# Kernel optimization log

Measured on AMD Instinct MI355X. Metric: run time of the kernel, lower is better.

## Reference

```python
import jax, jax.numpy as jnp
import numpy as np

B, T, E, D, OUT = 2048, 64, 256, 256, 2


def setup_inputs() -> dict:
    key = jax.random.key(0)
    ks = jax.random.split(key, 16)
    s = 0.05
    return {
        "input_encoded": jax.random.normal(ks[0], (B, T, E), dtype=jnp.float32),
        "y_history": jax.random.normal(ks[1], (B, T), dtype=jnp.float32),
        # attn_layer: Linear(2D+E -> E), Tanh, Linear(E -> 1)
        "W1": jax.random.normal(ks[2], (E, 2 * D + E), dtype=jnp.float32) * s,
        "b1": jax.random.normal(ks[3], (E,), dtype=jnp.float32) * s,
        "w2": jax.random.normal(ks[4], (E,), dtype=jnp.float32) * s,
        "b2": jax.random.normal(ks[5], (1,), dtype=jnp.float32) * s,
        # single-layer LSTM(input=OUT, hidden=D); gate order i,f,g,o
        "W_ih": jax.random.normal(ks[6], (4 * D, OUT), dtype=jnp.float32) * s,
        "b_ih": jax.random.normal(ks[7], (4 * D,), dtype=jnp.float32) * s,
        "W_hh": jax.random.normal(ks[8], (4 * D, D), dtype=jnp.float32) * s,
        "b_hh": jax.random.normal(ks[9], (4 * D,), dtype=jnp.float32) * s,
        # fc: Linear(E+T -> OUT) (torch init normal_() std=1; scaled here for stability)
        "W_fc": jax.random.normal(ks[10], (OUT, E + T), dtype=jnp.float32) * s,
        "b_fc": jax.random.normal(ks[11], (OUT,), dtype=jnp.float32) * s,
        # fc_final: Linear(D+E -> OUT)
        "W_final": jax.random.normal(ks[12], (OUT, D + E), dtype=jnp.float32) * s,
        "b_final": jax.random.normal(ks[13], (OUT,), dtype=jnp.float32) * s,
    }


def reference(input_encoded, y_history, W1, b1, w2, b2, W_ih, b_ih, W_hh, b_hh,
              W_fc, b_fc, W_final, b_final):
    Bs, Ts, Es = input_encoded.shape
    Ds = W_hh.shape[1]

    def step(carry, _):
        h, c, _ctx = carry  # h, c: [B, D]
        hc = jnp.concatenate([h, c], axis=-1)  # [B, 2D]
        hc_rep = jnp.broadcast_to(hc[:, None, :], (Bs, Ts, 2 * Ds))
        x = jnp.concatenate([hc_rep, input_encoded], axis=-1)  # [B, T, 2D+E]
        scores = jnp.tanh(x @ W1.T + b1) @ w2 + b2  # [B, T]
        alpha = jax.nn.softmax(scores, axis=1)
        ctx = jnp.einsum('bt,bte->be', alpha, input_encoded)  # [B, E]
        y_tilde = jnp.concatenate([ctx, y_history], axis=1) @ W_fc.T + b_fc  # [B, OUT]
        gates = y_tilde @ W_ih.T + b_ih + h @ W_hh.T + b_hh  # [B, 4D]
        i, f, g, o = jnp.split(gates, 4, axis=-1)
        c_new = jax.nn.sigmoid(f) * c + jax.nn.sigmoid(i) * jnp.tanh(g)
        h_new = jax.nn.sigmoid(o) * jnp.tanh(c_new)
        return (h_new, c_new, ctx), None

    init = (jnp.zeros((Bs, Ds), input_encoded.dtype),
            jnp.zeros((Bs, Ds), input_encoded.dtype),
            jnp.zeros((Bs, Es), input_encoded.dtype))
    (h, c, ctx), _ = jax.lax.scan(step, init, None, length=Ts)
    return jnp.concatenate([h, ctx], axis=1) @ W_final.T + b_final  # [B, OUT]
```

## Files before the change

### kernel.cpp

```cpp
#include <hip/hip_runtime.h>
#include <hip/hip_bf16.h>
#include <cstdint>
#include <cstddef>

#define LOG2E 1.44269504088896340736f

using f32x4 = __attribute__((ext_vector_type(4))) float;
using s16x8 = __attribute__((ext_vector_type(8))) short;

static __device__ __forceinline__ float bf2f(unsigned short u) {
  union { unsigned int i; float f; } v; v.i = ((unsigned int)u) << 16; return v.f;
}
static __device__ __forceinline__ unsigned short f2bf(float f) {
  union { float f; unsigned int i; } v; v.f = f;
  unsigned int r = v.i + 0x7fffu + ((v.i >> 16) & 1u);
  return (unsigned short)(r >> 16);
}
static __device__ __forceinline__ float wredmax(float v) {
  #pragma unroll
  for (int m = 32; m > 0; m >>= 1) v = fmaxf(v, __shfl_xor(v, m, 64));
  return v;
}
static __device__ __forceinline__ float wredsum(float v) {
  #pragma unroll
  for (int m = 32; m > 0; m >>= 1) v += __shfl_xor(v, m, 64);
  return v;
}

__global__ void ktrans(const float* __restrict__ W1, const float* __restrict__ b1,
                       const float* __restrict__ Wih_in, const float* __restrict__ bih,
                       const float* __restrict__ Whh, const float* __restrict__ bhh,
                       const float* __restrict__ Wfc, const float* __restrict__ bfc,
                       const float* __restrict__ yhist,
                       unsigned short* __restrict__ WB1, unsigned short* __restrict__ WBhh,
                       unsigned short* __restrict__ WB1e, float* __restrict__ b1s,
                       float* __restrict__ Wihs, float* __restrict__ gbias,
                       float* __restrict__ yh2)
{
  int idx = blockIdx.x * 256 + threadIdx.x;
  const float TS = 2.f * LOG2E;
  if (idx < 131072) {
    int k = idx >> 8, e = idx & 255;
    WB1[((k >> 3) * 256 + e) * 8 + (k & 7)] = f2bf(TS * W1[e * 768 + k]);
    return;
  }
  idx -= 131072;
  if (idx < 262144) {
    int k = idx >> 10, j = idx & 1023;
    float sc = ((j >> 8) == 2) ? TS : -LOG2E;
    WBhh[((k >> 3) * 1024 + j) * 8 + (k & 7)] = f2bf(sc * Whh[j * 256 + k]);
    return;
  }
  idx -= 262144;
  if (idx < 65536) {
    int k = idx >> 8, e = idx & 255;
    WB1e[((k >> 3) * 256 + e) * 8 + (k & 7)] = f2bf(TS * W1[e * 768 + 512 + k]);
    return;
  }
  idx -= 65536;
  if (idx < 256) { b1s[idx] = TS * b1[idx]; return; }
  idx -= 256;
  if (idx < 2048) {
    int j = idx >> 1;
    float sc = ((j >> 8) == 2) ? TS : -LOG2E;
    Wihs[idx] = sc * Wih_in[idx];
    return;
  }
  idx -= 2048;
  if (idx < 1024) {
    int j = idx;
    float sc = ((j >> 8) == 2) ? TS : -LOG2E;
    gbias[j] = sc * (bih[j] + bhh[j]);
    return;
  }
  idx -= 1024;
  if (idx < 4096) {
    int bq = idx >> 1, o = idx & 1;
    float a = bfc[o];
    for (int t = 0; t < 64; ++t) a = fmaf(yhist[bq * 64 + t], Wfc[o * 320 + 256 + t], a);
    yh2[idx] = a;
    return;
  }
}

__global__ __launch_bounds__(256, 4) void kpre(
    const float* __restrict__ x, const unsigned short* __restrict__ WB1e,
    const float* __restrict__ Wfc,
    unsigned short* __restrict__ P, float* __restrict__ ey)
{
  __shared__ __align__(16) unsigned short xs[16384];
  const int bq = blockIdx.x;
  const int tid = threadIdx.x;
  const int w = tid >> 6, lane = tid & 63;
  const float* __restrict__ xb = x + (size_t)bq * 16384;

  #pragma unroll 4
  for (int it = 0; it < 16; ++it) {
    int idx = it * 256 + tid;
    float4 v = *(const float4*)(xb + (size_t)idx * 4);
    int t = idx >> 6, e0 = (idx & 63) * 4;
    unsigned long long pk = (unsigned long long)f2bf(v.x)
        | ((unsigned long long)f2bf(v.y) << 16)
        | ((unsigned long long)f2bf(v.z) << 32)
        | ((unsigned long long)f2bf(v.w) << 48);
    int ba = (t * 512 + e0 * 2) ^ ((t & 7) << 4);
    *(unsigned long long*)((char*)xs + ba) = pk;
  }
  __syncthreads();

  const int mt = w;
  const int fgrp = lane >> 4, fcol = lane & 15;
  const int trow = mt * 16 + fcol;
  s16x8 af[8];
  #pragma unroll
  for (int kb = 0; kb < 8; ++kb) {
    int e = kb * 32 + fgrp * 8;
    int ba = (trow * 512 + e * 2) ^ ((trow & 7) << 4);
    af[kb] = *(const s16x8*)((char*)xs + ba);
  }
  __syncthreads();

  unsigned short* __restrict__ Pst = xs;
  #pragma unroll
  for (int nt = 0; nt < 16; ++nt) {
    s16x8 bfr[8];
    #pragma unroll
    for (int kb = 0; kb < 8; ++kb)
      bfr[kb] = *(const s16x8*)&WB1e[(size_t)((kb * 4 + fgrp) * 256 + nt * 16 + fcol) * 8];
    f32x4 acc = {0.f, 0.f, 0.f, 0.f};
    #pragma unroll
    for (int kb = 0; kb < 8; ++kb)
      acc = __builtin_amdgcn_mfma_f32_16x16x32_bf16(af[kb], bfr[kb], acc, 0, 0, 0);
    const int ep = nt * 16 + fcol;
    #pragma unroll
    for (int r = 0; r < 4; ++r)
      Pst[(mt * 16 + fgrp * 4 + r) * 256 + ep] = f2bf(acc[r]);
  }
  __syncthreads();

  unsigned int* __restrict__ Pd = (unsigned int*)(P + (size_t)bq * 16384);
  #pragma unroll 4
  for (int d = tid; d < 8192; d += 256) {
    int f = d * 2;
    int ec = f >> 9, t = (f >> 3) & 63, i0 = f & 7;
    unsigned int lo = Pst[t * 256 + ec * 8 + i0];
    unsigned int hi = Pst[t * 256 + ec * 8 + i0 + 1];
    Pd[d] = lo | (hi << 16);
  }

  if (tid < 128) {
    int t = tid >> 1, o = tid & 1;
    float a = 0.f;
    const float* __restrict__ xr = xb + t * 256;
    const float* __restrict__ wr = Wfc + o * 320;
    #pragma unroll 4
    for (int e = 0; e < 256; ++e) a = fmaf(xr[e], wr[e], a);
    ey[((size_t)bq * 64 + t) * 2 + o] = a;
  }
}

#define SIG(X) __builtin_amdgcn_rcpf(1.f + __builtin_amdgcn_exp2f(X))

#define SCCHUNK(PV, EC) do { \
  const float4 qa_ = *(const float4*)(qrow + (EC) * 8); \
  const float4 qc_ = *(const float4*)(qrow + (EC) * 8 + 4); \
  const float4 wa_ = *(const float4*)(w2f + (EC) * 8); \
  const float4 wc_ = *(const float4*)(w2f + (EC) * 8 + 4); \
  a0 = fmaf(wa_.x, SIG(bf2f((unsigned short)(PV)[0]) + qa_.x), a0); \
  a1 = fmaf(wa_.y, SIG(bf2f((unsigned short)(PV)[1]) + qa_.y), a1); \
  a2 = fmaf(wa_.z, SIG(bf2f((unsigned short)(PV)[2]) + qa_.z), a2); \
  a3 = fmaf(wa_.w, SIG(bf2f((unsigned short)(PV)[3]) + qa_.w), a3); \
  a0 = fmaf(wc_.x, SIG(bf2f((unsigned short)(PV)[4]) + qc_.x), a0); \
  a1 = fmaf(wc_.y, SIG(bf2f((unsigned short)(PV)[5]) + qc_.y), a1); \
  a2 = fmaf(wc_.z, SIG(bf2f((unsigned short)(PV)[6]) + qc_.z), a2); \
  a3 = fmaf(wc_.w, SIG(bf2f((unsigned short)(PV)[7]) + qc_.w), a3); \
} while (0)

#define SCL(EC) do { \
  const s16x8 pvL_ = *(const s16x8*)&Plds[b][(EC) - 16][lane][0]; \
  SCCHUNK(pvL_, EC); \
} while (0)

#define AH(KB) (*(const s16x8*)&hcA[(((KB) * 4 + fgrp) * 8 + frow) * 8])

#define GUNIT(U, S0, S1, S2, S3) do { \
  const size_t jb_ = (size_t)((((U) & 3) * 256 + ((U) >> 2) * 128 + w * 16 + fcol)) * 8; \
  const s16x8 wb0_ = *(const s16x8*)&WBhh[jb_ + (size_t)(0 * 4 + fgrp) * 8192]; \
  const s16x8 wb1_ = *(const s16x8*)&WBhh[jb_ + (size_t)(1 * 4 + fgrp) * 8192]; \
  const s16x8 wb2_ = *(const s16x8*)&WBhh[jb_ + (size_t)(2 * 4 + fgrp) * 8192]; \
  const s16x8 wb3_ = *(const s16x8*)&WBhh[jb_ + (size_t)(3 * 4 + fgrp) * 8192]; \
  const s16x8 wb4_ = *(const s16x8*)&WBhh[jb_ + (size_t)(4 * 4 + fgrp) * 8192]; \
  const s16x8 wb5_ = *(const s16x8*)&WBhh[jb_ + (size_t)(5 * 4 + fgrp) * 8192]; \
  const s16x8 wb6_ = *(const s16x8*)&WBhh[jb_ + (size_t)(6 * 4 + fgrp) * 8192]; \
  const s16x8 wb7_ = *(const s16x8*)&WBhh[jb_ + (size_t)(7 * 4 + fgrp) * 8192]; \
  G##U = (f32x4){gb_##U, gb_##U, gb_##U, gb_##U}; \
  S0; S1; S2; S3; \
  G##U = __builtin_amdgcn_mfma_f32_16x16x32_bf16(AH(0), wb0_, G##U, 0, 0, 0); \
  G##U = __builtin_amdgcn_mfma_f32_16x16x32_bf16(AH(1), wb1_, G##U, 0, 0, 0); \
  G##U = __builtin_amdgcn_mfma_f32_16x16x32_bf16(AH(2), wb2_, G##U, 0, 0, 0); \
  G##U = __builtin_amdgcn_mfma_f32_16x16x32_bf16(AH(3), wb3_, G##U, 0, 0, 0); \
  G##U = __builtin_amdgcn_mfma_f32_16x16x32_bf16(AH(4), wb4_, G##U, 0, 0, 0); \
  G##U = __builtin_amdgcn_mfma_f32_16x16x32_bf16(AH(5), wb5_, G##U, 0, 0, 0); \
  G##U = __builtin_amdgcn_mfma_f32_16x16x32_bf16(AH(6), wb6_, G##U, 0, 0, 0); \
  G##U = __builtin_amdgcn_mfma_f32_16x16x32_bf16(AH(7), wb7_, G##U, 0, 0, 0); \
} while (0)

#define PW(CG, R, CV, Gi, Gf, Gg, Go, w0i, w1i, w0f, w1f, w0g, w1g, w0o, w1o) do { \
  const int row_ = (drow0 + (R)) & 7; \
  const int jj_ = (CG) * 128 + w * 16 + fcol; \
  const float y0_ = yt[row_][0], y1_ = yt[row_][1]; \
  const float gi_ = (Gi)[R] + fmaf(w0i, y0_, (w1i) * y1_); \
  const float gf_ = (Gf)[R] + fmaf(w0f, y0_, (w1f) * y1_); \
  const float gg_ = (Gg)[R] + fmaf(w0g, y0_, (w1g) * y1_); \
  const float go_ = (Go)[R] + fmaf(w0o, y0_, (w1o) * y1_); \
  const float si_ = SIG(gi_); \
  const float sf_ = SIG(gf_); \
  const float tg_ = 1.f - 2.f * SIG(gg_); \
  const float so_ = SIG(go_); \
  const float cn_ = sf_ * (CV) + si_ * tg_; \
  (CV) = cn_; \
  const float th_ = 1.f - 2.f * SIG(2.f * LOG2E * cn_); \
  const float hn_ = so_ * th_; \
  if (lane < 32) { \
    hcA[((jj_ >> 3) * 8 + row_) * 8 + (jj_ & 7)] = f2bf(hn_); \
    hcA[((32 + (jj_ >> 3)) * 8 + row_) * 8 + (jj_ & 7)] = f2bf(cn_); \
    if (s == 63) qf[row_][jj_] = hn_; \
  } \
} while (0)

#define PLOADR(U) const s16x8 p##U = *(const s16x8*)(Pb + (size_t)((U) * 64 + lane) * 8);

#define WIGB(U) \
  const int j##U = (((U) & 3) * 256 + ((U) >> 2) * 128 + w * 16 + fcol); \
  const float wi0_##U = Wihs[2 * j##U]; \
  const float wi1_##U = Wihs[2 * j##U + 1]; \
  const float gb_##U = gbias[j##U];

__global__ __launch_bounds__(512, 1) void krecur(
    const float* __restrict__ x, const float* __restrict__ w2g,
    const unsigned short* __restrict__ WB1, const unsigned short* __restrict__ WBhh,
    const float* __restrict__ Wihs, const float* __restrict__ gbias,
    const float* __restrict__ b1s, const float* __restrict__ yh2,
    const float* __restrict__ ey, const unsigned short* __restrict__ P,
    const float* __restrict__ Wfin, const float* __restrict__ bfin,
    float* __restrict__ out)
{
  __shared__ __align__(16) unsigned short Plds[8][16][64][8];
  __shared__ __align__(16) unsigned short hcA[4096];
  __shared__ __align__(16) float qf[8][256];
  __shared__ __align__(16) float w2f[256];
  __shared__ __align__(16) float scAl[8][64];
  __shared__ float yt[8][2];

  const int tid = threadIdx.x;
  const int w = tid >> 6, lane = tid & 63;
  const int b = w;
  const int gbase = blockIdx.x * 8;
  const int gb = gbase + b;

  for (int i = tid; i < 4096; i += 512) hcA[i] = 0;
  if (tid < 256) w2f[tid] = w2g[tid];
  for (int i = tid; i < 8192; i += 512) {
    int row = i >> 10, rem = i & 1023, ec = rem >> 6, t = rem & 63;
    *(s16x8*)&Plds[row][ec][t][0] =
        *(const s16x8*)(P + (size_t)(gbase + row) * 16384 + (size_t)((16 + ec) * 64 + t) * 8);
  }

  const int frow = lane & 7;
  const int fgrp = lane >> 4;
  const int fcol = lane & 15;
  const int drow0 = fgrp * 4;

  const unsigned short* __restrict__ Pb = P + (size_t)gb * 16384;
  PLOADR(0)  PLOADR(1)  PLOADR(2)  PLOADR(3)
  PLOADR(4)  PLOADR(5)  PLOADR(6)  PLOADR(7)
  PLOADR(8)  PLOADR(9)  PLOADR(10) PLOADR(11)
  PLOADR(12) PLOADR(13) PLOADR(14) PLOADR(15)

  const float2 eyv = *(const float2*)(ey + ((size_t)gb * 64 + lane) * 2);
  const float yh0 = yh2[gb * 2], yh1 = yh2[gb * 2 + 1];
  const float b1r0 = b1s[(w * 2 + 0) * 16 + fcol];
  const float b1r1 = b1s[(w * 2 + 1) * 16 + fcol];

  WIGB(0) WIGB(1) WIGB(2) WIGB(3) WIGB(4) WIGB(5) WIGB(6) WIGB(7)

  float c0 = 0.f, c1 = 0.f, c2 = 0.f, c3 = 0.f;
  float c4 = 0.f, c5 = 0.f, c6 = 0.f, c7 = 0.f;

  __syncthreads();

  for (int s = 0; s < 64; ++s) {
    #pragma unroll
    for (int et2 = 0; et2 < 2; ++et2) {
      const int eb = (w * 2 + et2) * 16;
      f32x4 acc = {0.f, 0.f, 0.f, 0.f};
      #pragma unroll
      for (int kb = 0; kb < 16; ++kb) {
        const s16x8 bfr = *(const s16x8*)&WB1[(size_t)((kb * 4 + fgrp) * 256 + eb + fcol) * 8];
        acc = __builtin_amdgcn_mfma_f32_16x16x32_bf16(AH(kb), bfr, acc, 0, 0, 0);
      }
      if (lane < 32) {
        const float bb = et2 ? b1r1 : b1r0;
        #pragma unroll
        for (int r = 0; r < 4; ++r) qf[drow0 + r][eb + fcol] = acc[r] + bb;
      }
    }
    __syncthreads();

    float a0 = 0.f, a1 = 0.f, a2 = 0.f, a3 = 0.f;
    f32x4 G0, G1, G2, G3, G4, G5, G6, G7;
    const float* __restrict__ qrow = &qf[b][0];
    GUNIT(0, SCCHUNK(p0, 0),  SCCHUNK(p1, 1),  SCCHUNK(p2, 2),  SCCHUNK(p3, 3));
    GUNIT(1, SCCHUNK(p4, 4),  SCCHUNK(p5, 5),  SCCHUNK(p6, 6),  SCCHUNK(p7, 7));
    GUNIT(2, SCCHUNK(p8, 8),  SCCHUNK(p9, 9),  SCCHUNK(p10, 10), SCCHUNK(p11, 11));
    GUNIT(3, SCCHUNK(p12, 12), SCCHUNK(p13, 13), SCCHUNK(p14, 14), SCCHUNK(p15, 15));
    GUNIT(4, SCL(16), SCL(17), SCL(18), SCL(19));
    GUNIT(5, SCL(20), SCL(21), SCL(22), SCL(23));
    GUNIT(6, SCL(24), SCL(25), SCL(26), SCL(27));
    GUNIT(7, SCL(28), SCL(29), SCL(30), SCL(31));

    {
      float sc = -2.f * ((a0 + a1) + (a2 + a3));
      float mx = wredmax(sc);
      float e_t = __builtin_amdgcn_exp2f((sc - mx) * LOG2E);
      float sm = wredsum(e_t);
      float alpha = e_t * __builtin_amdgcn_rcpf(sm);
      if (s == 63) scAl[b][lane] = alpha;
      float y0 = wredsum(alpha * eyv.x);
      float y1 = wredsum(alpha * eyv.y);
      if (lane == 0) { yt[b][0] = y0 + yh0; yt[b][1] = y1 + yh1; }
    }
    __syncthreads();

    PW(0, 0, c0, G0, G1, G2, G3, wi0_0, wi1_0, wi0_1, wi1_1, wi0_2, wi1_2, wi0_3, wi1_3);
    PW(0, 1, c1, G0, G1, G2, G3, wi0_0, wi1_0, wi0_1, wi1_1, wi0_2, wi1_2, wi0_3, wi1_3);
    PW(0, 2, c2, G0, G1, G2, G3, wi0_0, wi1_0, wi0_1, wi1_1, wi0_2, wi1_2, wi0_3, wi1_3);
    PW(0, 3, c3, G0, G1, G2, G3, wi0_0, wi1_0, wi0_1, wi1_1, wi0_2, wi1_2, wi0_3, wi1_3);
    PW(1, 0, c4, G4, G5, G6, G7, wi0_4, wi1_4, wi0_5, wi1_5, wi0_6, wi1_6, wi0_7, wi1_7);
    PW(1, 1, c5, G4, G5, G6, G7, wi0_4, wi1_4, wi0_5, wi1_5, wi0_6, wi1_6, wi0_7, wi1_7);
    PW(1, 2, c6, G4, G5, G6, G7, wi0_4, wi1_4, wi0_5, wi1_5, wi0_6, wi1_6, wi0_7, wi1_7);
    PW(1, 3, c7, G4, G5, G6, G7, wi0_4, wi1_4, wi0_5, wi1_5, wi0_6, wi1_6, wi0_7, wi1_7);
    __syncthreads();

    if (s == 63) {
      float* __restrict__ ctxS = (float*)Plds;
      #pragma unroll
      for (int p = 0; p < 4; ++p) {
        const int e = p * 64 + lane;
        float a = 0.f;
        const float* __restrict__ xr = x + (size_t)gb * 16384 + e;
        #pragma unroll 8
        for (int t = 0; t < 64; ++t) a = fmaf(scAl[b][t], xr[t * 256], a);
        ctxS[b * 256 + e] = a;
      }
      __syncthreads();
    }
  }

  {
    const float* __restrict__ ctxS = (const float*)Plds;
    float o0 = 0.f, o1 = 0.f;
    #pragma unroll
    for (int kk = 0; kk < 8; ++kk) {
      const int k = kk * 64 + lane;
      const float v = (k < 256) ? qf[b][k] : ctxS[b * 256 + (k - 256)];
      o0 = fmaf(v, Wfin[k], o0);
      o1 = fmaf(v, Wfin[512 + k], o1);
    }
    o0 = wredsum(o0);
    o1 = wredsum(o1);
    if (lane == 0) {
      out[gb * 2 + 0] = o0 + bfin[0];
      out[gb * 2 + 1] = o1 + bfin[1];
    }
  }
}

extern "C" void kernel_launch(void* const* d_in, const int* in_sizes, int n_in,
                              void* d_out, int out_size, void* d_ws, size_t ws_size,
                              hipStream_t stream) {
  const float* x    = (const float*)d_in[0];
  const float* yh   = (const float*)d_in[1];
  const float* W1   = (const float*)d_in[2];
  const float* b1   = (const float*)d_in[3];
  const float* w2   = (const float*)d_in[4];
  const float* Wih  = (const float*)d_in[6];
  const float* bih  = (const float*)d_in[7];
  const float* Whh  = (const float*)d_in[8];
  const float* bhh  = (const float*)d_in[9];
  const float* Wfc  = (const float*)d_in[10];
  const float* bfc  = (const float*)d_in[11];
  const float* Wfin = (const float*)d_in[12];
  const float* bfin = (const float*)d_in[13];

  char* ws = (char*)d_ws;
  unsigned short* P    = (unsigned short*)(ws + 0);
  unsigned short* WB1  = (unsigned short*)(ws + 67108864);
  unsigned short* WBhh = (unsigned short*)(ws + 67371008);
  unsigned short* WB1e = (unsigned short*)(ws + 67895296);
  float* b1s   = (float*)(ws + 68026368);
  float* Wihs  = (float*)(ws + 68027392);
  float* gbias = (float*)(ws + 68035584);
  float* yh2   = (float*)(ws + 68039680);
  float* ey    = (float*)(ws + 68056064);

  ktrans<<<1821, 256, 0, stream>>>(W1, b1, Wih, bih, Whh, bhh, Wfc, bfc, yh,
                                   WB1, WBhh, WB1e, b1s, Wihs, gbias, yh2);
  kpre<<<2048, 256, 0, stream>>>(x, WB1e, Wfc, P, ey);
  krecur<<<256, 512, 0, stream>>>(x, w2, WB1, WBhh, Wihs, gbias, b1s, yh2, ey, P,
                                  Wfin, bfin, (float*)d_out);
}
```

Baseline: 3.880 ms.

## Stream half of P from global each step instead of holding it in registers

The first 16 chunks of the per-row precomputed P tile are no longer kept in 16 persistent s16x8 registers. They are reloaded each step with nontemporal global loads. The MFMA gate units are also moved ahead of the score computation instead of being interleaved with it, and the launch-bounds minimum-blocks hint is dropped. The aim is to lower register pressure and simplify scheduling, at the cost of re-reading about 16 KB per row from global/L2 on every one of the 64 steps and losing the MFMA/VALU interleave.

Result: slower. 4.600 ms (+18.6%).

```diff
diff --git a/kernel.cpp b/kernel.cpp
--- a/kernel.cpp
+++ b/kernel.cpp
@@ -176,6 +176,9 @@
   a3 = fmaf(wc_.w, SIG(bf2f((unsigned short)(PV)[7]) + qc_.w), a3); \
 } while (0)
 
+#define PNT(EC) const s16x8 pn##EC = \
+  __builtin_nontemporal_load((const s16x8*)(Pb + (size_t)(EC) * 512 + lane * 8));
+
 #define SCL(EC) do { \
   const s16x8 pvL_ = *(const s16x8*)&Plds[b][(EC) - 16][lane][0]; \
   SCCHUNK(pvL_, EC); \
@@ -183,7 +186,7 @@
 
 #define AH(KB) (*(const s16x8*)&hcA[(((KB) * 4 + fgrp) * 8 + frow) * 8])
 
-#define GUNIT(U, S0, S1, S2, S3) do { \
+#define GUNIT(U) do { \
   const size_t jb_ = (size_t)((((U) & 3) * 256 + ((U) >> 2) * 128 + w * 16 + fcol)) * 8; \
   const s16x8 wb0_ = *(const s16x8*)&WBhh[jb_ + (size_t)(0 * 4 + fgrp) * 8192]; \
   const s16x8 wb1_ = *(const s16x8*)&WBhh[jb_ + (size_t)(1 * 4 + fgrp) * 8192]; \
@@ -194,7 +197,6 @@
   const s16x8 wb6_ = *(const s16x8*)&WBhh[jb_ + (size_t)(6 * 4 + fgrp) * 8192]; \
   const s16x8 wb7_ = *(const s16x8*)&WBhh[jb_ + (size_t)(7 * 4 + fgrp) * 8192]; \
   G##U = (f32x4){gb_##U, gb_##U, gb_##U, gb_##U}; \
-  S0; S1; S2; S3; \
   G##U = __builtin_amdgcn_mfma_f32_16x16x32_bf16(AH(0), wb0_, G##U, 0, 0, 0); \
   G##U = __builtin_amdgcn_mfma_f32_16x16x32_bf16(AH(1), wb1_, G##U, 0, 0, 0); \
   G##U = __builtin_amdgcn_mfma_f32_16x16x32_bf16(AH(2), wb2_, G##U, 0, 0, 0); \
@@ -228,15 +230,13 @@
   } \
 } while (0)
 
-#define PLOADR(U) const s16x8 p##U = *(const s16x8*)(Pb + (size_t)((U) * 64 + lane) * 8);
-
 #define WIGB(U) \
   const int j##U = (((U) & 3) * 256 + ((U) >> 2) * 128 + w * 16 + fcol); \
   const float wi0_##U = Wihs[2 * j##U]; \
   const float wi1_##U = Wihs[2 * j##U + 1]; \
   const float gb_##U = gbias[j##U];
 
-__global__ __launch_bounds__(512, 1) void krecur(
+__global__ __launch_bounds__(512) void krecur(
     const float* __restrict__ x, const float* __restrict__ w2g,
     const unsigned short* __restrict__ WB1, const unsigned short* __restrict__ WBhh,
     const float* __restrict__ Wihs, const float* __restrict__ gbias,
@@ -262,8 +262,9 @@
   if (tid < 256) w2f[tid] = w2g[tid];
   for (int i = tid; i < 8192; i += 512) {
     int row = i >> 10, rem = i & 1023, ec = rem >> 6, t = rem & 63;
-    *(s16x8*)&Plds[row][ec][t][0] =
-        *(const s16x8*)(P + (size_t)(gbase + row) * 16384 + (size_t)((16 + ec) * 64 + t) * 8);
+    const s16x8 v = __builtin_nontemporal_load(
+        (const s16x8*)(P + (size_t)(gbase + row) * 16384 + (size_t)((16 + ec) * 64 + t) * 8));
+    *(s16x8*)&Plds[row][ec][t][0] = v;
   }
 
   const int frow = lane & 7;
@@ -272,10 +273,6 @@
   const int drow0 = fgrp * 4;
 
   const unsigned short* __restrict__ Pb = P + (size_t)gb * 16384;
-  PLOADR(0)  PLOADR(1)  PLOADR(2)  PLOADR(3)
-  PLOADR(4)  PLOADR(5)  PLOADR(6)  PLOADR(7)
-  PLOADR(8)  PLOADR(9)  PLOADR(10) PLOADR(11)
-  PLOADR(12) PLOADR(13) PLOADR(14) PLOADR(15)
 
   const float2 eyv = *(const float2*)(ey + ((size_t)gb * 64 + lane) * 2);
   const float yh0 = yh2[gb * 2], yh1 = yh2[gb * 2 + 1];
@@ -307,17 +304,26 @@
     }
     __syncthreads();
 
+    f32x4 G0, G1, G2, G3, G4, G5, G6, G7;
+    GUNIT(0); GUNIT(1); GUNIT(2); GUNIT(3);
+    GUNIT(4); GUNIT(5); GUNIT(6); GUNIT(7);
+
     float a0 = 0.f, a1 = 0.f, a2 = 0.f, a3 = 0.f;
-    f32x4 G0, G1, G2, G3, G4, G5, G6, G7;
     const float* __restrict__ qrow = &qf[b][0];
-    GUNIT(0, SCCHUNK(p0, 0),  SCCHUNK(p1, 1),  SCCHUNK(p2, 2),  SCCHUNK(p3, 3));
-    GUNIT(1, SCCHUNK(p4, 4),  SCCHUNK(p5, 5),  SCCHUNK(p6, 6),  SCCHUNK(p7, 7));
-    GUNIT(2, SCCHUNK(p8, 8),  SCCHUNK(p9, 9),  SCCHUNK(p10, 10), SCCHUNK(p11, 11));
-    GUNIT(3, SCCHUNK(p12, 12), SCCHUNK(p13, 13), SCCHUNK(p14, 14), SCCHUNK(p15, 15));
-    GUNIT(4, SCL(16), SCL(17), SCL(18), SCL(19));
-    GUNIT(5, SCL(20), SCL(21), SCL(22), SCL(23));
-    GUNIT(6, SCL(24), SCL(25), SCL(26), SCL(27));
-    GUNIT(7, SCL(28), SCL(29), SCL(30), SCL(31));
+    {
+      PNT(0) PNT(1) PNT(2) PNT(3) PNT(4) PNT(5) PNT(6) PNT(7)
+      SCCHUNK(pn0, 0); SCCHUNK(pn1, 1); SCCHUNK(pn2, 2); SCCHUNK(pn3, 3);
+      SCCHUNK(pn4, 4); SCCHUNK(pn5, 5); SCCHUNK(pn6, 6); SCCHUNK(pn7, 7);
+    }
+    {
+      PNT(8) PNT(9) PNT(10) PNT(11) PNT(12) PNT(13) PNT(14) PNT(15)
+      SCCHUNK(pn8, 8);   SCCHUNK(pn9, 9);   SCCHUNK(pn10, 10); SCCHUNK(pn11, 11);
+      SCCHUNK(pn12, 12); SCCHUNK(pn13, 13); SCCHUNK(pn14, 14); SCCHUNK(pn15, 15);
+    }
+    SCL(16); SCL(17); SCL(18); SCL(19);
+    SCL(20); SCL(21); SCL(22); SCL(23);
+    SCL(24); SCL(25); SCL(26); SCL(27);
+    SCL(28); SCL(29); SCL(30); SCL(31);
 
     {
       float sc = -2.f * ((a0 + a1) + (a2 + a3));
```
